# Kernel tuning notes

Hardware: AMD Instinct MI355X
Metric: run time of the kernel (lower is better)

The kernel has to match this reference:

```python
import jax, jax.numpy as jnp
import numpy as np

N = 50000          # nodes (ogbn-products-like subgraph)
E = 800000         # directed edges (avg degree 16)
F_IN, HID, HEADS, OUT = 100, 32, 4, 47
W1 = HID * HEADS   # 128
NEG_SLOPE = 0.2
BN_EPS = 1e-5


def _gatv2(x, src, dst, w_src, w_dst, att, bias, heads, ch):
    """GATv2Conv (PyG semantics, share_weights=False, concat).
    x: [N, F]; src/dst: [Etot] (self-loops already appended);
    w_src/w_dst: [F, heads*ch]; att: [heads, ch]; bias: [heads*ch].
    """
    n = x.shape[0]
    xl = (x @ w_src).reshape(n, heads, ch)   # source-side transform
    xr = (x @ w_dst).reshape(n, heads, ch)   # target-side transform
    # per-edge attention logits: a . leaky_relu(xl[j] + xr[i])  -> [E, heads]
    e = jnp.sum(jax.nn.leaky_relu(xl[src] + xr[dst], NEG_SLOPE) * att, axis=-1)
    # segment softmax over incoming edges of each destination node
    m = jax.ops.segment_max(e, dst, num_segments=n)          # [N, heads]
    ex = jnp.exp(e - m[dst])
    denom = jax.ops.segment_sum(ex, dst, num_segments=n)     # [N, heads]
    alpha = ex / denom[dst]                                  # [E, heads]
    # weighted scatter-add aggregation of source features
    out = jax.ops.segment_sum(alpha[:, :, None] * xl[src], dst, num_segments=n)
    return out.reshape(n, heads * ch) + bias


def _bn_eval(x, g, b, m, v):
    return (x - m) * jax.lax.rsqrt(v + BN_EPS) * g + b


def setup_inputs() -> dict:
    key = jax.random.key(0)
    ks = jax.random.split(key, 32)
    s = 0.1
    inp = {
        "x": jax.random.normal(ks[0], (N, F_IN), jnp.float32),
        "edge_index": jax.random.randint(ks[1], (2, E), 0, N, dtype=jnp.int32),
        "w1_src": jax.random.normal(ks[2], (F_IN, W1), jnp.float32) * s,
        "w1_dst": jax.random.normal(ks[3], (F_IN, W1), jnp.float32) * s,
        "att1": jax.random.normal(ks[4], (HEADS, HID), jnp.float32) * s,
        "b1": jnp.zeros((W1,), jnp.float32),
        "bn1_g": jnp.ones((W1,), jnp.float32),
        "bn1_b": jnp.zeros((W1,), jnp.float32),
        "bn1_m": jax.random.normal(ks[5], (W1,), jnp.float32) * 0.05,
        "bn1_v": jax.random.uniform(ks[6], (W1,), jnp.float32, 0.5, 1.5),
        "res0_w": jax.random.normal(ks[7], (F_IN, W1), jnp.float32) * s,
        "res0_b": jnp.zeros((W1,), jnp.float32),
        "w2_src": jax.random.normal(ks[8], (W1, W1), jnp.float32) * s,
        "w2_dst": jax.random.normal(ks[9], (W1, W1), jnp.float32) * s,
        "att2": jax.random.normal(ks[10], (HEADS, HID), jnp.float32) * s,
        "b2": jnp.zeros((W1,), jnp.float32),
        "bn2_g": jnp.ones((W1,), jnp.float32),
        "bn2_b": jnp.zeros((W1,), jnp.float32),
        "bn2_m": jax.random.normal(ks[11], (W1,), jnp.float32) * 0.05,
        "bn2_v": jax.random.uniform(ks[12], (W1,), jnp.float32, 0.5, 1.5),
        # layer 3: 128 -> 47, heads=1
        "w3_src": jax.random.normal(ks[13], (W1, OUT), jnp.float32) * s,
        "w3_dst": jax.random.normal(ks[14], (W1, OUT), jnp.float32) * s,
        "att3": jax.random.normal(ks[15], (1, OUT), jnp.float32) * s,
        "b3": jnp.zeros((OUT,), jnp.float32),
        "bn3_g": jnp.ones((OUT,), jnp.float32),
        "bn3_b": jnp.zeros((OUT,), jnp.float32),
        "bn3_m": jax.random.normal(ks[16], (OUT,), jnp.float32) * 0.05,
        "bn3_v": jax.random.uniform(ks[17], (OUT,), jnp.float32, 0.5, 1.5),
        "res2_w": jax.random.normal(ks[18], (W1, OUT), jnp.float32) * s,
        "res2_b": jnp.zeros((OUT,), jnp.float32),
    }
    return inp


def reference(x, edge_index,
              w1_src, w1_dst, att1, b1, bn1_g, bn1_b, bn1_m, bn1_v, res0_w, res0_b,
              w2_src, w2_dst, att2, b2, bn2_g, bn2_b, bn2_m, bn2_v,
              w3_src, w3_dst, att3, b3, bn3_g, bn3_b, bn3_m, bn3_v, res2_w, res2_b):
    # add self-loops (PyG GATv2Conv default add_self_loops=True)
    loops = jnp.arange(x.shape[0], dtype=edge_index.dtype)
    src = jnp.concatenate([edge_index[0], loops])
    dst = jnp.concatenate([edge_index[1], loops])

    # layer 1 + linear residual + BN + relu (eval mode: no dropout)
    h = _gatv2(x, src, dst, w1_src, w1_dst, att1, b1, HEADS, HID)
    h = h + (x @ res0_w + res0_b)
    h = jax.nn.relu(_bn_eval(h, bn1_g, bn1_b, bn1_m, bn1_v))

    # layer 2 + identity residual + BN + relu
    h2 = _gatv2(h, src, dst, w2_src, w2_dst, att2, b2, HEADS, HID)
    h2 = h2 + h
    h2 = jax.nn.relu(_bn_eval(h2, bn2_g, bn2_b, bn2_m, bn2_v))

    # layer 3 (heads=1) + linear residual + BN (no relu/dropout on last layer)
    out = _gatv2(h2, src, dst, w3_src, w3_dst, att3, b3, 1, OUT)
    out = out + (h2 @ res2_w + res2_b)
    out = _bn_eval(out, bn3_g, bn3_b, bn3_m, bn3_v)
    return out
```

## Files before the change

kernel.cpp:

```cpp
#include <hip/hip_runtime.h>
#include <math.h>

#define BN_EPS 1e-5f
#define SLOT 96
#define LN16 2.7725887f
#define BCAP 5120

typedef _Float16 h2 __attribute__((ext_vector_type(2)));
typedef _Float16 h4 __attribute__((ext_vector_type(4)));
typedef _Float16 h8 __attribute__((ext_vector_type(8)));
typedef float f2v __attribute__((ext_vector_type(2)));
typedef float float4v __attribute__((ext_vector_type(4)));

static __device__ inline h2 bit_h2(unsigned u) {
    union { unsigned u; h2 h; } c; c.u = u; return c.h;
}
static __device__ inline unsigned bit_u(h2 h) {
    union { unsigned u; h2 h; } c; c.h = h; return c.u;
}

template <int CTRL>
static __device__ inline float dpp_add(float x) {
    int y = __builtin_amdgcn_update_dpp(0, __float_as_int(x), CTRL, 0xF, 0xF, true);
    return x + __int_as_float(y);
}
static __device__ inline float red8_dpp(float t) {
    t = dpp_add<0xB1>(t); t = dpp_add<0x4E>(t); t = dpp_add<0x141>(t);
    return t;
}
static __device__ inline float red16_dpp(float t) {
    t = dpp_add<0xB1>(t); t = dpp_add<0x4E>(t); t = dpp_add<0x141>(t);
    t = dpp_add<0x140>(t);
    return t;
}

static __device__ inline void pack_one(int idx,
                                       const float* p0, const float* p1,
                                       const float* p2,
                                       int w0, int w1, int w2,
                                       int Ksrc, int Ncat,
                                       _Float16* out) {
    int k = idx / Ncat, n = idx - k * Ncat;
    float v = 0.f;
    if (k < Ksrc) {
        if (n < w0) v = p0[(size_t)k * w0 + n];
        else if (n < w0 + w1) v = p1[(size_t)k * w1 + (n - w0)];
        else if (w2 > 0 && n < w0 + w1 + w2) v = p2[(size_t)k * w2 + (n - w0 - w1)];
    }
    int kt = k >> 5, kr = k & 31;
    int quad = kr >> 3, j = kr & 7;
    int nt = n >> 4, nr = n & 15;
    int ntiles = Ncat >> 4;
    out[((size_t)(kt * ntiles + nt) * 64 + quad * 16 + nr) * 8 + j] = (_Float16)v;
}

__global__ __launch_bounds__(256) void prep_bin_k(
    const int* __restrict__ src, const int* __restrict__ dst, int E, int Etot,
    int* __restrict__ gcnt, int* __restrict__ bbuf, int nbA,
    const float* __restrict__ x, _Float16* __restrict__ A, int N,
    const float* __restrict__ w1s, const float* __restrict__ w1d,
    const float* __restrict__ r0w, const float* __restrict__ w2s,
    const float* __restrict__ w2d, const float* __restrict__ w3s,
    const float* __restrict__ w3d, const float* __restrict__ r2w,
    _Float16* __restrict__ Wb1, _Float16* __restrict__ Wb2,
    _Float16* __restrict__ Wb3) {
    if ((int)blockIdx.x < nbA) {
        __shared__ int hist[256];
        __shared__ int base[256];
        int tid = threadIdx.x;
        hist[tid] = 0;
        __syncthreads();
        int per = (Etot + nbA - 1) / nbA;
        int e0 = blockIdx.x * per;
        int e1 = min(e0 + per, Etot);
        for (int i = e0 + tid; i < e1; i += 256) {
            int d = (i < E) ? dst[i] : (i - E);
            atomicAdd(&hist[d >> 8], 1);
        }
        __syncthreads();
        int h = hist[tid];
        if (h) base[tid] = atomicAdd(&gcnt[tid], h);
        __syncthreads();
        for (int i = e0 + tid; i < e1; i += 256) {
            int d = (i < E) ? dst[i] : (i - E);
            int s = (i < E) ? src[i] : (i - E);
            int b = d >> 8;
            int off = atomicAdd(&base[b], 1);
            if (off < BCAP) bbuf[(size_t)b * BCAP + off] = ((d & 255) << 16) | s;
        }
        return;
    }
    const int S1 = 128 * 384, S2 = 128 * 256, S3 = 128 * 144;
    int convTot = N * 32;
    int idx = (blockIdx.x - nbA) * 256 + threadIdx.x;
    if (idx < convTot) {
        int n = idx >> 5, t = idx & 31;
        float4 v = {0.f, 0.f, 0.f, 0.f};
        if (t < 25) v = *(const float4*)(x + (size_t)n * 100 + t * 4);
        h4 o = {(_Float16)v.x, (_Float16)v.y, (_Float16)v.z, (_Float16)v.w};
        *(h4*)(A + (size_t)n * 128 + t * 4) = o;
        return;
    }
    int p = idx - convTot;
    if (p < S1) pack_one(p, w1s, w1d, r0w, 128, 128, 128, 100, 384, Wb1);
    else if (p < S1 + S2) pack_one(p - S1, w2s, w2d, nullptr, 128, 128, 0, 128, 256, Wb2);
    else if (p < S1 + S2 + S3) pack_one(p - S1 - S2, w3s, w3d, r2w, 47, 47, 47, 128, 144, Wb3);
}

template <int NT>
__global__ __launch_bounds__(256) void mfma_gemm(const _Float16* __restrict__ A,
                                                 const _Float16* __restrict__ Bp,
                                                 _Float16* __restrict__ XLR,
                                                 float* __restrict__ RES,
                                                 int M, int Ncat,
                                                 int ncat_valid, int res_off,
                                                 int bf_remap, int bf_shift,
                                                 int bf_stride, int res_stride,
                                                 const int* __restrict__ gcnt,
                                                 const int* __restrict__ bbuf,
                                                 int* __restrict__ esrc,
                                                 int* __restrict__ cnt,
                                                 int scatN, int Nn) {
    __shared__ int lcnt[256];
    int bid = blockIdx.x;
    if (bid < scatN) {
        int tid = threadIdx.x;
        lcnt[tid] = 0;
        __syncthreads();
        int cb = gcnt[bid];
        if (cb > BCAP) cb = BCAP;
        const int* bp = bbuf + (size_t)bid * BCAP;
        int b0 = bid << 8;
        for (int i = tid; i < cb; i += 256) {
            int w = bp[i];
            int dl = (w >> 16) & 255;
            int s = w & 0xFFFF;
            int pos = atomicAdd(&lcnt[dl], 1);
            esrc[(size_t)(b0 + dl) * SLOT + pos] = s << 9;
        }
        __syncthreads();
        int d = b0 + tid;
        if (d < Nn) cnt[d] = lcnt[tid];
        return;
    }
    int mt = ((bid - scatN) * 256 + threadIdx.x) >> 6;
    int lane = threadIdx.x & 63;
    int mtiles = M >> 4;
    if (mt >= mtiles) return;
    int ngroups = Ncat / (16 * NT);
    int ntiles = Ncat >> 4;
    int quad = lane >> 4;
    int nr = lane & 15;
    int row = mt * 16 + nr;

    h8 a[4];
#pragma unroll
    for (int kt = 0; kt < 4; kt++)
        a[kt] = *(const h8*)(A + (size_t)row * 128 + kt * 32 + quad * 8);

    int rowb = mt * 16 + quad * 4;
    for (int ng = 0; ng < ngroups; ng++) {
        float4v acc[NT];
#pragma unroll
        for (int t = 0; t < NT; t++) acc[t] = (float4v){0.f, 0.f, 0.f, 0.f};
#pragma unroll
        for (int kt = 0; kt < 4; kt++) {
            const _Float16* bbase =
                Bp + ((size_t)(kt * ntiles + ng * NT) * 64 + lane) * 8;
#pragma unroll
            for (int t = 0; t < NT; t++) {
                h8 b = *(const h8*)(bbase + (size_t)t * 512);
                acc[t] = __builtin_amdgcn_mfma_f32_16x16x32_f16(a[kt], b, acc[t], 0, 0, 0);
            }
        }
#pragma unroll
        for (int t = 0; t < NT; t++) {
            int col = (ng * NT + t) * 16 + nr;
            if (col >= ncat_valid) continue;
            if (col < res_off) {
                int bc = (col >= bf_remap) ? col + bf_shift : col;
#pragma unroll
                for (int r = 0; r < 4; r++)
                    XLR[(size_t)(rowb + r) * bf_stride + bc] = (_Float16)acc[t][r];
            } else {
                int rc = col - res_off;
#pragma unroll
                for (int r = 0; r < 4; r++)
                    RES[(size_t)(rowb + r) * res_stride + rc] = acc[t][r];
            }
        }
    }
}

static __device__ inline void edge8(uint2 u, h2 xr01, h2 xr23, h2 at01,
                                    h2 at23, float& den, h2& acc01, h2& acc23,
                                    float gate) {
    const h2 NS = {(_Float16)0.2f, (_Float16)0.2f};
    h2 a01 = bit_h2(u.x), a23 = bit_h2(u.y);
    h2 v01 = a01 + xr01, v23 = a23 + xr23;
    v01 = __builtin_elementwise_max(v01, v01 * NS);
    v23 = __builtin_elementwise_max(v23, v23 * NS);
    h2 t2 = v01 * at01 + v23 * at23;
    f2v tf = __builtin_convertvector(t2, f2v);
    float t = red8_dpp(tf.x + tf.y);
    float p = __expf(t - LN16) * gate;
    den += p;
    h2 P = {(_Float16)p, (_Float16)p};
    acc01 = P * a01 + acc01;
    acc23 = P * a23 + acc23;
}
static __device__ inline void edge16(uint2 u, h2 xr01, h2 xr23, h2 at01,
                                     h2 at23, float& den, h2& acc01,
                                     h2& acc23, float gate) {
    const h2 NS = {(_Float16)0.2f, (_Float16)0.2f};
    h2 a01 = bit_h2(u.x), a23 = bit_h2(u.y);
    h2 v01 = a01 + xr01, v23 = a23 + xr23;
    v01 = __builtin_elementwise_max(v01, v01 * NS);
    v23 = __builtin_elementwise_max(v23, v23 * NS);
    h2 t2 = v01 * at01 + v23 * at23;
    f2v tf = __builtin_convertvector(t2, f2v);
    float t = red16_dpp(tf.x + tf.y);
    float p = __expf(t - LN16) * gate;
    den += p;
    h2 P = {(_Float16)p, (_Float16)p};
    acc01 = P * a01 + acc01;
    acc23 = P * a23 + acc23;
}

__global__ __launch_bounds__(256) void gat_agg4_gemm(
    const int* __restrict__ cnt, const int* __restrict__ esrc,
    const _Float16* __restrict__ xlr,
    const float* __restrict__ att,
    const float* __restrict__ RES,
    const _Float16* __restrict__ hprev,
    const float* __restrict__ resB, const float* __restrict__ bias,
    const float* __restrict__ g, const float* __restrict__ bb,
    const float* __restrict__ mm, const float* __restrict__ vv,
    _Float16* __restrict__ hout,
    const _Float16* __restrict__ Bp,
    _Float16* __restrict__ XLRo, float* __restrict__ RESo,
    int Ncat, int ncat_valid, int res_off, int bf_remap, int bf_shift,
    int bf_stride, int res_stride,
    int N, int mode) {
    __shared__ _Float16 hT[16][136];
    int d0 = blockIdx.x * 16;
    int wv = threadIdx.x >> 6;
    int lane = threadIdx.x & 63;
    int half = lane >> 5;
    int gl = lane & 31;
    int c0 = gl * 4;
    const char* xb = (const char*)xlr + c0 * 2;

    float4 af = *(const float4*)(att + c0);
    h2 at01 = {(_Float16)af.x, (_Float16)af.y};
    h2 at23 = {(_Float16)af.z, (_Float16)af.w};
    float4 bi = *(const float4*)(bias + c0);
    float4 gm = *(const float4*)(mm + c0);
    float4 gv = *(const float4*)(vv + c0);
    float4 gg = *(const float4*)(g + c0);
    float4 gb = *(const float4*)(bb + c0);
    float4 rb = {0.f, 0.f, 0.f, 0.f};
    if (mode == 1) rb = *(const float4*)(resB + c0);

    int myoff4[4], cnt4[4];
#pragma unroll
    for (int i = 0; i < 4; i++) {
        int dd = d0 + (wv << 2) + i;
        dd = dd < N ? dd : N - 1;
        cnt4[i] = cnt[dd];
        myoff4[i] = esrc[(size_t)dd * SLOT + lane];
    }

#pragma unroll
    for (int i = 0; i < 4; i++) {
        int d = d0 + (wv << 2) + i;
        int dd = d < N ? d : N - 1;
        int beg = dd * SLOT;
        int cnt_d = cnt4[i];
        int myoff = myoff4[i];

        uint2 xrv = *(const uint2*)(xb + (size_t)dd * 512 + 256);
        h2 xr01 = bit_h2(xrv.x), xr23 = bit_h2(xrv.y);
        float4 rres = {0.f, 0.f, 0.f, 0.f};
        uint2 hpv = {0u, 0u};
        if (mode == 1) rres = *(const float4*)(RES + (size_t)dd * 128 + c0);
        else hpv = *(const uint2*)(hprev + (size_t)dd * 128 + c0);

        int K = (cnt_d + 1) >> 1;
        int KB = K < 12 ? K : 12;
        uint2 u[12];
#pragma unroll
        for (int k = 0; k < 12; k++) {
            if (k < KB) {
                int ee = 2 * k + half;
                int ec = ee < cnt_d ? ee : 0;
                int o = __shfl(myoff, ec);
                u[k] = *(const uint2*)(xb + o);
            }
        }
        float den = 0.f;
        h2 acc01 = {(_Float16)0.f, (_Float16)0.f};
        h2 acc23 = acc01;
#pragma unroll
        for (int k = 0; k < 12; k++) {
            if (k < KB) {
                int ee = 2 * k + half;
                edge8(u[k], xr01, xr23, at01, at23, den, acc01, acc23,
                      ee < cnt_d ? 1.f : 0.f);
            }
        }
        for (int e = 24; e < cnt_d; e += 2) {
            int ee = e + half;
            bool act = ee < cnt_d;
            int ec = act ? ee : cnt_d - 1;
            int o = __shfl(myoff, ec < 64 ? ec : 0);
            if (ec >= 64) o = esrc[beg + ec];
            uint2 u0 = *(const uint2*)(xb + o);
            edge8(u0, xr01, xr23, at01, at23, den, acc01, acc23,
                  act ? 1.f : 0.f);
        }
        den += __shfl_xor(den, 32);
        f2v c01 = __builtin_convertvector(acc01, f2v);
        f2v c23 = __builtin_convertvector(acc23, f2v);
        float f0 = c01.x, f1 = c01.y, fA = c23.x, fB = c23.y;
        f0 += __shfl_xor(f0, 32);
        f1 += __shfl_xor(f1, 32);
        fA += __shfl_xor(fA, 32);
        fB += __shfl_xor(fB, 32);

        if (half == 0) {
            float inv = 1.f / den;
            float o0 = f0 * inv + bi.x;
            float o1 = f1 * inv + bi.y;
            float o2 = fA * inv + bi.z;
            float o3 = fB * inv + bi.w;
            if (mode == 1) {
                o0 += rres.x + rb.x; o1 += rres.y + rb.y;
                o2 += rres.z + rb.z; o3 += rres.w + rb.w;
            } else {
                f2v g01 = __builtin_convertvector(bit_h2(hpv.x), f2v);
                f2v g23 = __builtin_convertvector(bit_h2(hpv.y), f2v);
                o0 += g01.x; o1 += g01.y; o2 += g23.x; o3 += g23.y;
            }
            o0 = fmaxf((o0 - gm.x) * rsqrtf(gv.x + BN_EPS) * gg.x + gb.x, 0.f);
            o1 = fmaxf((o1 - gm.y) * rsqrtf(gv.y + BN_EPS) * gg.y + gb.y, 0.f);
            o2 = fmaxf((o2 - gm.z) * rsqrtf(gv.z + BN_EPS) * gg.z + gb.z, 0.f);
            o3 = fmaxf((o3 - gm.w) * rsqrtf(gv.w + BN_EPS) * gg.w + gb.w, 0.f);
            h2 s01 = {(_Float16)o0, (_Float16)o1};
            h2 s23 = {(_Float16)o2, (_Float16)o3};
            uint2 w;
            w.x = bit_u(s01);
            w.y = bit_u(s23);
            int lr = (wv << 2) + i;
            *(uint2*)(&hT[lr][c0]) = w;
            if (mode == 1 && d < N)
                *(uint2*)(hout + (size_t)d * 128 + c0) = w;
        }
    }
    __syncthreads();

    int quad = lane >> 4;
    int nr = lane & 15;
    h8 a[4];
#pragma unroll
    for (int kt = 0; kt < 4; kt++)
        a[kt] = *(const h8*)(&hT[nr][kt * 32 + quad * 8]);

    int ntiles = Ncat >> 4;
    for (int t = wv; t < ntiles; t += 4) {
        float4v acc = (float4v){0.f, 0.f, 0.f, 0.f};
#pragma unroll
        for (int kt = 0; kt < 4; kt++) {
            h8 b = *(const h8*)(Bp + ((size_t)(kt * ntiles + t) * 64 + lane) * 8);
            acc = __builtin_amdgcn_mfma_f32_16x16x32_f16(a[kt], b, acc, 0, 0, 0);
        }
        int col = t * 16 + nr;
        if (col >= ncat_valid) continue;
        if (col < res_off) {
            int bc = (col >= bf_remap) ? col + bf_shift : col;
#pragma unroll
            for (int r = 0; r < 4; r++) {
                int grow = d0 + quad * 4 + r;
                if (grow < N)
                    XLRo[(size_t)grow * bf_stride + bc] = (_Float16)acc[r];
            }
        } else {
            int rc = col - res_off;
#pragma unroll
            for (int r = 0; r < 4; r++) {
                int grow = d0 + quad * 4 + r;
                if (grow < N)
                    RESo[(size_t)grow * res_stride + rc] = acc[r];
            }
        }
    }
}

__global__ __launch_bounds__(256) void gat_agg1_fused(
    const int* __restrict__ cnt, const int* __restrict__ esrc,
    const _Float16* __restrict__ xlr, const float* __restrict__ att,
    const float* __restrict__ RES, const float* __restrict__ resB,
    const float* __restrict__ bias,
    const float* __restrict__ g, const float* __restrict__ bb,
    const float* __restrict__ mm, const float* __restrict__ vv,
    float* __restrict__ out, int N) {
    int d = blockIdx.x * 4 + (threadIdx.x >> 6);
    if (d >= N) return;
    int lane = threadIdx.x & 63;
    int gl = lane & 15, grp = lane >> 4;
    const char* xb = (const char*)xlr + gl * 8;

    int beg = d * SLOT;
    int cnt_d = cnt[d];
    int myoff = esrc[beg + lane];

    uint2 xrv = *(const uint2*)(xb + (size_t)d * 512 + 128);
    float4 rres = *(const float4*)(RES + (size_t)d * 128 + gl * 4);

    h2 xr01 = bit_h2(xrv.x), xr23 = bit_h2(xrv.y);
    float atf[4];
#pragma unroll
    for (int k = 0; k < 4; k++) {
        int c = gl * 4 + k;
        atf[k] = (c < 47) ? att[c] : 0.f;
    }
    h2 at01 = {(_Float16)atf[0], (_Float16)atf[1]};
    h2 at23 = {(_Float16)atf[2], (_Float16)atf[3]};

    int nmain = cnt_d < 64 ? cnt_d : 64;
    int nb1 = nmain < 48 ? nmain : 48;
    int K1 = (nb1 + 3) >> 2;
    uint2 u[12];
#pragma unroll
    for (int k = 0; k < 12; k++) {
        if (k < K1) {
            int idx = grp + 4 * k;
            int ec = idx < nmain ? idx : 0;
            int o = __shfl(myoff, ec);
            u[k] = *(const uint2*)(xb + o);
        }
    }
    float den = 0.f;
    h2 acc01 = {(_Float16)0.f, (_Float16)0.f};
    h2 acc23 = acc01;
#pragma unroll
    for (int k = 0; k < 12; k++) {
        if (k < K1) {
            int idx = grp + 4 * k;
            edge16(u[k], xr01, xr23, at01, at23, den, acc01, acc23,
                   idx < nmain ? 1.f : 0.f);
        }
    }
    for (int ibase = 48; ibase < nmain; ibase += 4) {
        int idx = ibase + grp;
        bool act = idx < nmain;
        int o = __shfl(myoff, act ? idx : 0);
        uint2 u0 = *(const uint2*)(xb + o);
        edge16(u0, xr01, xr23, at01, at23, den, acc01, acc23, act ? 1.f : 0.f);
    }
    for (int j = beg + 64 + grp; j < beg + cnt_d; j += 4) {
        int o = esrc[j];
        uint2 u0 = *(const uint2*)(xb + o);
        edge16(u0, xr01, xr23, at01, at23, den, acc01, acc23, 1.f);
    }
    den += __shfl_xor(den, 16);
    den += __shfl_xor(den, 32);
    f2v c01 = __builtin_convertvector(acc01, f2v);
    f2v c23 = __builtin_convertvector(acc23, f2v);
    float f[4] = {c01.x, c01.y, c23.x, c23.y};
#pragma unroll
    for (int k = 0; k < 4; k++) {
        f[k] += __shfl_xor(f[k], 16);
        f[k] += __shfl_xor(f[k], 32);
    }
    if (grp == 0 && gl < 12) {
        float inv = 1.f / den;
        float rr[4] = {rres.x, rres.y, rres.z, rres.w};
#pragma unroll
        for (int k = 0; k < 4; k++) {
            int c = gl * 4 + k;
            if (c < 47) {
                float o = f[k] * inv + bias[c] + rr[k] + resB[c];
                o = (o - mm[c]) * rsqrtf(vv[c] + BN_EPS) * g[c] + bb[c];
                out[(size_t)d * 47 + c] = o;
            }
        }
    }
}

extern "C" void kernel_launch(void* const* d_in, const int* in_sizes, int n_in,
                              void* d_out, int out_size, void* d_ws, size_t ws_size,
                              hipStream_t stream) {
    const float* x      = (const float*)d_in[0];
    const int*   ei     = (const int*)d_in[1];
    const float* w1_src = (const float*)d_in[2];
    const float* w1_dst = (const float*)d_in[3];
    const float* att1   = (const float*)d_in[4];
    const float* b1     = (const float*)d_in[5];
    const float* bn1_g  = (const float*)d_in[6];
    const float* bn1_b  = (const float*)d_in[7];
    const float* bn1_m  = (const float*)d_in[8];
    const float* bn1_v  = (const float*)d_in[9];
    const float* res0_w = (const float*)d_in[10];
    const float* res0_b = (const float*)d_in[11];
    const float* w2_src = (const float*)d_in[12];
    const float* w2_dst = (const float*)d_in[13];
    const float* att2   = (const float*)d_in[14];
    const float* b2     = (const float*)d_in[15];
    const float* bn2_g  = (const float*)d_in[16];
    const float* bn2_b  = (const float*)d_in[17];
    const float* bn2_m  = (const float*)d_in[18];
    const float* bn2_v  = (const float*)d_in[19];
    const float* w3_src = (const float*)d_in[20];
    const float* w3_dst = (const float*)d_in[21];
    const float* att3   = (const float*)d_in[22];
    const float* b3     = (const float*)d_in[23];
    const float* bn3_g  = (const float*)d_in[24];
    const float* bn3_b  = (const float*)d_in[25];
    const float* bn3_m  = (const float*)d_in[26];
    const float* bn3_v  = (const float*)d_in[27];
    const float* res2_w = (const float*)d_in[28];
    const float* res2_b = (const float*)d_in[29];

    const int F_IN = 100;
    const int KP = 128;
    const int NC1 = 384, NC2 = 256, NC3 = 144;
    int N = in_sizes[0] / F_IN;
    int E = in_sizes[1] / 2;
    int Etot = E + N;
    const int* src = ei;
    const int* dst = ei + E;
    int nbuck = (N + 255) >> 8;

    float* ws = (float*)d_ws;
    size_t o = 0;
    _Float16* XLR = (_Float16*)(ws + o); o += (size_t)N * 128;
    float* B_res = ws + o; o += (size_t)N * 128;
    _Float16* A_h = (_Float16*)(ws + o); o += (size_t)N * 64;
    _Float16* Wb1 = (_Float16*)(ws + o); o += (size_t)KP * NC1 / 2;
    _Float16* Wb2 = (_Float16*)(ws + o); o += (size_t)KP * NC2 / 2;
    _Float16* Wb3 = (_Float16*)(ws + o); o += (size_t)KP * NC3 / 2;
    int* I_cnt  = (int*)(ws + o); o += N;
    int* I_esrc = (int*)(ws + o); o += (size_t)N * SLOT + 4;
    int* I_gcnt = (int*)(ws + o); o += 256;
    int* I_bbuf = (int*)(ws + o); o += (size_t)nbuck * BCAP;
    (void)ws_size; (void)n_in; (void)out_size;

    int mtiles = (N + 15) / 16;
    int agg16Grid = (N + 15) / 16;
    int aggGrid = (N + 3) / 4;
    int gemmGrid = (mtiles + 3) / 4;

    hipMemsetAsync(I_gcnt, 0, 256 * sizeof(int), stream);

    {
        int nbA = 512;
        int convTot = N * 32;
        int packTot = KP * (NC1 + NC2 + NC3);
        int pb = (convTot + packTot + 255) / 256;
        prep_bin_k<<<nbA + pb, 256, 0, stream>>>(
            src, dst, E, Etot, I_gcnt, I_bbuf, nbA, x, A_h, N,
            w1_src, w1_dst, res0_w, w2_src, w2_dst, w3_src, w3_dst, res2_w,
            Wb1, Wb2, Wb3);
    }

    mfma_gemm<4><<<nbuck + gemmGrid, 256, 0, stream>>>(
        A_h, Wb1, XLR, B_res, N, NC1, 384, 256, 384, 0, 256, 128,
        I_gcnt, I_bbuf, I_esrc, I_cnt, nbuck, N);

    gat_agg4_gemm<<<agg16Grid, 256, 0, stream>>>(
        I_cnt, I_esrc, XLR, att1, B_res, nullptr, res0_b, b1,
        bn1_g, bn1_b, bn1_m, bn1_v, A_h,
        Wb2, (_Float16*)B_res, nullptr,
        NC2, 256, 256, 384, 0, 256, 0,
        N, 1);

    gat_agg4_gemm<<<agg16Grid, 256, 0, stream>>>(
        I_cnt, I_esrc, (const _Float16*)B_res, att2, nullptr, A_h, nullptr, b2,
        bn2_g, bn2_b, bn2_m, bn2_v, nullptr,
        Wb3, XLR, (float*)XLR + 64,
        NC3, 141, 94, 47, 17, 256, 128,
        N, 2);

    gat_agg1_fused<<<aggGrid, 256, 0, stream>>>(
        I_cnt, I_esrc, XLR, att3, (const float*)((float*)XLR + 64), res2_b, b3,
        bn3_g, bn3_b, bn3_m, bn3_v, (float*)d_out, N);
}
```

Before: 327.5 us.

## Assign one wavefront per destination node in fused GAT aggregation kernel

Moves the fused layer-1/2 aggregation+GEMM kernel from 4 waves each handling 4 destination nodes to 16 waves (1024 threads) each handling one node. The aim is more independent gathers in flight and shorter per-wave serial chains, with the follow-on MFMA tile loop striding over 16 waves. The trade-offs are a larger block that may cap occupancy or registers under launch_bounds(1024), and BN parameter loads and A-fragment loads now issued per tile iteration.

```diff
diff --git a/kernel.cpp b/kernel.cpp
--- a/kernel.cpp
+++ b/kernel.cpp
@@ -227,7 +227,7 @@
     acc23 = P * a23 + acc23;
 }
 
-__global__ __launch_bounds__(256) void gat_agg4_gemm(
+__global__ __launch_bounds__(1024) void gat_agg4_gemm(
     const int* __restrict__ cnt, const int* __restrict__ esrc,
     const _Float16* __restrict__ xlr,
     const float* __restrict__ att,
@@ -251,123 +251,111 @@
     int c0 = gl * 4;
     const char* xb = (const char*)xlr + c0 * 2;
 
+    int d = d0 + wv;
+    int dd = d < N ? d : N - 1;
+    int beg = dd * SLOT;
+    int cnt_d = cnt[dd];
+    int myoff = esrc[(size_t)beg + lane];
+
     float4 af = *(const float4*)(att + c0);
     h2 at01 = {(_Float16)af.x, (_Float16)af.y};
     h2 at23 = {(_Float16)af.z, (_Float16)af.w};
     float4 bi = *(const float4*)(bias + c0);
-    float4 gm = *(const float4*)(mm + c0);
-    float4 gv = *(const float4*)(vv + c0);
-    float4 gg = *(const float4*)(g + c0);
-    float4 gb = *(const float4*)(bb + c0);
+    float4 rres = {0.f, 0.f, 0.f, 0.f};
+    uint2 hpv = {0u, 0u};
     float4 rb = {0.f, 0.f, 0.f, 0.f};
-    if (mode == 1) rb = *(const float4*)(resB + c0);
-
-    int myoff4[4], cnt4[4];
-#pragma unroll
-    for (int i = 0; i < 4; i++) {
-        int dd = d0 + (wv << 2) + i;
-        dd = dd < N ? dd : N - 1;
-        cnt4[i] = cnt[dd];
-        myoff4[i] = esrc[(size_t)dd * SLOT + lane];
-    }
-
-#pragma unroll
-    for (int i = 0; i < 4; i++) {
-        int d = d0 + (wv << 2) + i;
-        int dd = d < N ? d : N - 1;
-        int beg = dd * SLOT;
-        int cnt_d = cnt4[i];
-        int myoff = myoff4[i];
-
-        uint2 xrv = *(const uint2*)(xb + (size_t)dd * 512 + 256);
-        h2 xr01 = bit_h2(xrv.x), xr23 = bit_h2(xrv.y);
-        float4 rres = {0.f, 0.f, 0.f, 0.f};
-        uint2 hpv = {0u, 0u};
-        if (mode == 1) rres = *(const float4*)(RES + (size_t)dd * 128 + c0);
-        else hpv = *(const uint2*)(hprev + (size_t)dd * 128 + c0);
-
-        int K = (cnt_d + 1) >> 1;
-        int KB = K < 12 ? K : 12;
-        uint2 u[12];
-#pragma unroll
-        for (int k = 0; k < 12; k++) {
-            if (k < KB) {
-                int ee = 2 * k + half;
-                int ec = ee < cnt_d ? ee : 0;
-                int o = __shfl(myoff, ec);
-                u[k] = *(const uint2*)(xb + o);
-            }
-        }
-        float den = 0.f;
-        h2 acc01 = {(_Float16)0.f, (_Float16)0.f};
-        h2 acc23 = acc01;
-#pragma unroll
-        for (int k = 0; k < 12; k++) {
-            if (k < KB) {
-                int ee = 2 * k + half;
-                edge8(u[k], xr01, xr23, at01, at23, den, acc01, acc23,
-                      ee < cnt_d ? 1.f : 0.f);
-            }
-        }
-        for (int e = 24; e < cnt_d; e += 2) {
-            int ee = e + half;
-            bool act = ee < cnt_d;
-            int ec = act ? ee : cnt_d - 1;
-            int o = __shfl(myoff, ec < 64 ? ec : 0);
-            if (ec >= 64) o = esrc[beg + ec];
-            uint2 u0 = *(const uint2*)(xb + o);
-            edge8(u0, xr01, xr23, at01, at23, den, acc01, acc23,
-                  act ? 1.f : 0.f);
-        }
-        den += __shfl_xor(den, 32);
-        f2v c01 = __builtin_convertvector(acc01, f2v);
-        f2v c23 = __builtin_convertvector(acc23, f2v);
-        float f0 = c01.x, f1 = c01.y, fA = c23.x, fB = c23.y;
-        f0 += __shfl_xor(f0, 32);
-        f1 += __shfl_xor(f1, 32);
-        fA += __shfl_xor(fA, 32);
-        fB += __shfl_xor(fB, 32);
-
-        if (half == 0) {
-            float inv = 1.f / den;
-            float o0 = f0 * inv + bi.x;
-            float o1 = f1 * inv + bi.y;
-            float o2 = fA * inv + bi.z;
-            float o3 = fB * inv + bi.w;
-            if (mode == 1) {
-                o0 += rres.x + rb.x; o1 += rres.y + rb.y;
-                o2 += rres.z + rb.z; o3 += rres.w + rb.w;
-            } else {
-                f2v g01 = __builtin_convertvector(bit_h2(hpv.x), f2v);
-                f2v g23 = __builtin_convertvector(bit_h2(hpv.y), f2v);
-                o0 += g01.x; o1 += g01.y; o2 += g23.x; o3 += g23.y;
-            }
-            o0 = fmaxf((o0 - gm.x) * rsqrtf(gv.x + BN_EPS) * gg.x + gb.x, 0.f);
-            o1 = fmaxf((o1 - gm.y) * rsqrtf(gv.y + BN_EPS) * gg.y + gb.y, 0.f);
-            o2 = fmaxf((o2 - gm.z) * rsqrtf(gv.z + BN_EPS) * gg.z + gb.z, 0.f);
-            o3 = fmaxf((o3 - gm.w) * rsqrtf(gv.w + BN_EPS) * gg.w + gb.w, 0.f);
-            h2 s01 = {(_Float16)o0, (_Float16)o1};
-            h2 s23 = {(_Float16)o2, (_Float16)o3};
-            uint2 w;
-            w.x = bit_u(s01);
-            w.y = bit_u(s23);
-            int lr = (wv << 2) + i;
-            *(uint2*)(&hT[lr][c0]) = w;
-            if (mode == 1 && d < N)
-                *(uint2*)(hout + (size_t)d * 128 + c0) = w;
-        }
+    if (mode == 1) {
+        rres = *(const float4*)(RES + (size_t)dd * 128 + c0);
+        rb = *(const float4*)(resB + c0);
+    } else {
+        hpv = *(const uint2*)(hprev + (size_t)dd * 128 + c0);
+    }
+
+    uint2 xrv = *(const uint2*)(xb + (size_t)dd * 512 + 256);
+    h2 xr01 = bit_h2(xrv.x), xr23 = bit_h2(xrv.y);
+
+    int K = (cnt_d + 1) >> 1;
+    int KB = K < 12 ? K : 12;
+    uint2 u[12];
+#pragma unroll
+    for (int k = 0; k < 12; k++) {
+        if (k < KB) {
+            int ee = 2 * k + half;
+            int ec = ee < cnt_d ? ee : 0;
+            int o = __shfl(myoff, ec);
+            u[k] = *(const uint2*)(xb + o);
+        }
+    }
+    float den = 0.f;
+    h2 acc01 = {(_Float16)0.f, (_Float16)0.f};
+    h2 acc23 = acc01;
+#pragma unroll
+    for (int k = 0; k < 12; k++) {
+        if (k < KB) {
+            int ee = 2 * k + half;
+            edge8(u[k], xr01, xr23, at01, at23, den, acc01, acc23,
+                  ee < cnt_d ? 1.f : 0.f);
+        }
+    }
+    for (int e = 24; e < cnt_d; e += 2) {
+        int ee = e + half;
+        bool act = ee < cnt_d;
+        int ec = act ? ee : cnt_d - 1;
+        int o = __shfl(myoff, ec < 64 ? ec : 0);
+        if (ec >= 64) o = esrc[beg + ec];
+        uint2 u0 = *(const uint2*)(xb + o);
+        edge8(u0, xr01, xr23, at01, at23, den, acc01, acc23, act ? 1.f : 0.f);
+    }
+    den += __shfl_xor(den, 32);
+    f2v c01 = __builtin_convertvector(acc01, f2v);
+    f2v c23 = __builtin_convertvector(acc23, f2v);
+    float f0 = c01.x, f1 = c01.y, fA = c23.x, fB = c23.y;
+    f0 += __shfl_xor(f0, 32);
+    f1 += __shfl_xor(f1, 32);
+    fA += __shfl_xor(fA, 32);
+    fB += __shfl_xor(fB, 32);
+
+    if (half == 0) {
+        float4 gm = *(const float4*)(mm + c0);
+        float4 gv = *(const float4*)(vv + c0);
+        float4 gg = *(const float4*)(g + c0);
+        float4 gb = *(const float4*)(bb + c0);
+        float inv = 1.f / den;
+        float o0 = f0 * inv + bi.x;
+        float o1 = f1 * inv + bi.y;
+        float o2 = fA * inv + bi.z;
+        float o3 = fB * inv + bi.w;
+        if (mode == 1) {
+            o0 += rres.x + rb.x; o1 += rres.y + rb.y;
+            o2 += rres.z + rb.z; o3 += rres.w + rb.w;
+        } else {
+            f2v g01 = __builtin_convertvector(bit_h2(hpv.x), f2v);
+            f2v g23 = __builtin_convertvector(bit_h2(hpv.y), f2v);
+            o0 += g01.x; o1 += g01.y; o2 += g23.x; o3 += g23.y;
+        }
+        o0 = fmaxf((o0 - gm.x) * rsqrtf(gv.x + BN_EPS) * gg.x + gb.x, 0.f);
+        o1 = fmaxf((o1 - gm.y) * rsqrtf(gv.y + BN_EPS) * gg.y + gb.y, 0.f);
+        o2 = fmaxf((o2 - gm.z) * rsqrtf(gv.z + BN_EPS) * gg.z + gb.z, 0.f);
+        o3 = fmaxf((o3 - gm.w) * rsqrtf(gv.w + BN_EPS) * gg.w + gb.w, 0.f);
+        h2 s01 = {(_Float16)o0, (_Float16)o1};
+        h2 s23 = {(_Float16)o2, (_Float16)o3};
+        uint2 w;
+        w.x = bit_u(s01);
+        w.y = bit_u(s23);
+        *(uint2*)(&hT[wv][c0]) = w;
+        if (mode == 1 && d < N)
+            *(uint2*)(hout + (size_t)d * 128 + c0) = w;
     }
     __syncthreads();
 
     int quad = lane >> 4;
     int nr = lane & 15;
-    h8 a[4];
-#pragma unroll
-    for (int kt = 0; kt < 4; kt++)
-        a[kt] = *(const h8*)(&hT[nr][kt * 32 + quad * 8]);
-
     int ntiles = Ncat >> 4;
-    for (int t = wv; t < ntiles; t += 4) {
+    for (int t = wv; t < ntiles; t += 16) {
+        h8 a[4];
+#pragma unroll
+        for (int kt = 0; kt < 4; kt++)
+            a[kt] = *(const h8*)(&hT[nr][kt * 32 + quad * 8]);
         float4v acc = (float4v){0.f, 0.f, 0.f, 0.f};
 #pragma unroll
         for (int kt = 0; kt < 4; kt++) {
@@ -568,14 +556,14 @@
         A_h, Wb1, XLR, B_res, N, NC1, 384, 256, 384, 0, 256, 128,
         I_gcnt, I_bbuf, I_esrc, I_cnt, nbuck, N);
 
-    gat_agg4_gemm<<<agg16Grid, 256, 0, stream>>>(
+    gat_agg4_gemm<<<agg16Grid, 1024, 0, stream>>>(
         I_cnt, I_esrc, XLR, att1, B_res, nullptr, res0_b, b1,
         bn1_g, bn1_b, bn1_m, bn1_v, A_h,
         Wb2, (_Float16*)B_res, nullptr,
         NC2, 256, 256, 384, 0, 256, 0,
         N, 1);
 
-    gat_agg4_gemm<<<agg16Grid, 256, 0, stream>>>(
+    gat_agg4_gemm<<<agg16Grid, 1024, 0, stream>>>(
         I_cnt, I_esrc, (const _Float16*)B_res, att2, nullptr, A_h, nullptr, b2,
         bn2_g, bn2_b, bn2_m, bn2_v, nullptr,
         Wb3, XLR, (float*)XLR + 64,
```

Result: slower. 370.5 us (+13.1%).
